# Performance work log

Hardware: AMD Instinct MI355X
Metric: run time of the kernel (lower is better)

Reference implementation:

```python
import jax, jax.numpy as jnp
import numpy as np

B, S, D = 1, 1024, 4096
N_HEADS, N_KV, HEAD_DIM = 32, 8, 128
ALPHA = 5.0
BUDGET = 0.2
NEG = -10000.0


def rotate_half(x):
    x1 = x[..., : x.shape[-1] // 2]
    x2 = x[..., x.shape[-1] // 2 :]
    return jnp.concatenate((-x2, x1), axis=-1)


def kv_cache_mask(scores):
    # scores: [b, h, T, S]. Faithful vectorized version of the torch per-row
    # topk/scatter loop (capacity=1.0 => eviction loop body never executes).
    b, h, T, Ssrc = scores.shape
    attn = scores.reshape(b * h, T, Ssrc)
    causal_add = jnp.triu(jnp.full((T, Ssrc), NEG, scores.dtype), 1)
    attn = attn + causal_add
    # torch: torch.max(attn, -1, keepdim=True)[0][0] -> row maxes of head 0 only
    max_val = jnp.max(attn[0], axis=-1, keepdims=True)  # [T, 1]
    fetch_num = jnp.sum(attn >= (max_val - ALPHA), axis=-1)  # [BH, T]
    fetch_num = jnp.mean(fetch_num.astype(scores.dtype), axis=0).astype(jnp.int32)  # [T]
    fetch_max = int(Ssrc * BUDGET)
    fetch_num = jnp.minimum(fetch_num, fetch_max)
    # rank of every column within its (row-causal-masked) row, descending score
    order = jnp.argsort(-attn, axis=-1)           # [BH, T, S]
    ranks = jnp.argsort(order, axis=-1)           # [BH, T, S]
    rows = jnp.arange(T)
    keep_topk = ranks < fetch_num[None, :, None]  # variable-k topk per row
    tril = jnp.arange(Ssrc)[None, :] <= rows[:, None]  # dense causal rows
    fetch = jnp.where((rows < fetch_max)[None, :, None], tril[None], keep_topk)
    mask = jnp.where(fetch, 0.0, NEG).astype(scores.dtype).reshape(b, h, T, Ssrc)
    density = fetch.astype(jnp.float32).sum() / (b * h) / (T * (T + 1) / 2)
    return mask, density


def setup_inputs() -> dict:
    key = jax.random.key(0)
    ks = jax.random.split(key, 5)
    hidden_states = jax.random.normal(ks[0], (B, S, D), jnp.float32)
    # standard RoPE tables, theta=10000
    inv_freq = 1.0 / (10000.0 ** (np.arange(0, HEAD_DIM, 2, dtype=np.float64) / HEAD_DIM))
    freqs = np.outer(np.arange(S, dtype=np.float64), inv_freq)  # [S, hd/2]
    emb = np.concatenate([freqs, freqs], axis=-1)               # [S, hd]
    cos = jnp.asarray(np.cos(emb), jnp.float32)[None]           # [1, S, hd]
    sin = jnp.asarray(np.sin(emb), jnp.float32)[None]
    Wq = jax.random.normal(ks[1], (N_HEADS * HEAD_DIM, D), jnp.float32) * 0.02
    Wk = jax.random.normal(ks[2], (N_KV * HEAD_DIM, D), jnp.float32) * 0.02
    Wv = jax.random.normal(ks[3], (N_KV * HEAD_DIM, D), jnp.float32) * 0.02
    Wo = jax.random.normal(ks[4], (D, N_HEADS * HEAD_DIM), jnp.float32) * 0.02
    return {"hidden_states": hidden_states, "cos": cos, "sin": sin,
            "Wq": Wq, "Wk": Wk, "Wv": Wv, "Wo": Wo}


def reference(hidden_states, cos, sin, Wq, Wk, Wv, Wo):
    b, s, d = hidden_states.shape
    scaling = HEAD_DIM ** -0.5
    q = (hidden_states @ Wq.T).reshape(b, s, N_HEADS, HEAD_DIM).transpose(0, 2, 1, 3)
    k = (hidden_states @ Wk.T).reshape(b, s, N_KV, HEAD_DIM).transpose(0, 2, 1, 3)
    v = (hidden_states @ Wv.T).reshape(b, s, N_KV, HEAD_DIM).transpose(0, 2, 1, 3)
    c = cos[:, None]  # [b, 1, s, hd]
    sn = sin[:, None]
    q = q * c + rotate_half(q) * sn
    k = k * c + rotate_half(k) * sn
    n_rep = N_HEADS // N_KV
    k = jnp.repeat(k, n_rep, axis=1)
    v = jnp.repeat(v, n_rep, axis=1)
    scores = jnp.einsum("bhqd,bhkd->bhqk", q, k) * scaling
    mask, _density = kv_cache_mask(scores)
    probs = jax.nn.softmax(scores + mask, axis=-1)
    out = jnp.einsum("bhqk,bhkd->bhqd", probs, v)
    out = out.transpose(0, 2, 1, 3).reshape(b, s, N_HEADS * HEAD_DIM)
    return out @ Wo.T
```

## Files before the change

kernel.cpp:

```cpp
#include <hip/hip_runtime.h>
#include <hip/hip_bf16.h>
#include <hip/hip_fp16.h>

typedef unsigned int u32;
typedef unsigned short u16;
typedef __bf16 bf16x8 __attribute__((ext_vector_type(8)));
typedef float floatx4 __attribute__((ext_vector_type(4)));

#define SCALE 0.08838834764831845f
#define FETCH_MAX 204

__device__ __forceinline__ float bf2f(u16 u) {
    union { u32 i; float f; } v; v.i = ((u32)u) << 16; return v.f;
}
__device__ __forceinline__ u16 f2bf(float f) {
    union { float f; u32 i; } v; v.f = f;
    u32 r = v.i + 0x7FFFu + ((v.i >> 16) & 1u);
    return (u16)(r >> 16);
}
__device__ __forceinline__ u16 f2h_bits(float f) {
    __half h = __float2half(f);
    union { __half h; u16 u; } v; v.h = h; return v.u;
}
__device__ __forceinline__ float h_bits2f(u16 u) {
    union { __half h; u16 u; } v; v.u = u; return __half2float(v.h);
}
__device__ __forceinline__ u32 h2key(u16 hb) {
    return (u32)(u16)(hb ^ ((hb & 0x8000u) ? 0xFFFFu : 0x8000u));
}
__device__ __forceinline__ u16 key2h(u32 k) {
    return (u16)((k & 0x8000u) ? (k ^ 0x8000u) : (k ^ 0xFFFFu));
}

__global__ void detect_k(const u32* cosw, int* flag) {
    if (threadIdx.x == 0 && blockIdx.x == 0)
        *flag = (cosw[0] == 0x3F800000u) ? 1 : 0;
}

__global__ __launch_bounds__(256) void zero_k(int* p, int n) {
    int i = blockIdx.x * 256 + threadIdx.x;
    if (i < n) p[i] = 0;
}

__global__ __launch_bounds__(256) void convert_k(
    const int* flagp, const float* hs, const float* wq, const float* wk,
    const float* wv, const float* wo,
    u16* chs, u16* cwq, u16* cwk, u16* cwv, u16* cwo)
{
    if (*flagp == 0) return;
    const long S0 = 4194304/4, S1 = 16777216/4, S2 = 4194304/4, S3 = 4194304/4, S4 = 16777216/4;
    const long total = S0+S1+S2+S3+S4;
    for (long idx = (long)blockIdx.x*256 + threadIdx.x; idx < total; idx += (long)gridDim.x*256) {
        const float* src; u16* dst; long o = idx;
        if (o < S0)            { src = hs; dst = chs; }
        else if ((o -= S0) < S1) { src = wq; dst = cwq; }
        else if ((o -= S1) < S2) { src = wk; dst = cwk; }
        else if ((o -= S2) < S3) { src = wv; dst = cwv; }
        else                   { o -= S3; src = wo; dst = cwo; }
        float4 v = ((const float4*)src)[o];
        u32 lo = (u32)f2bf(v.x) | ((u32)f2bf(v.y) << 16);
        u32 hi = (u32)f2bf(v.z) | ((u32)f2bf(v.w) << 16);
        ((uint2*)dst)[o] = make_uint2(lo, hi);
    }
}

__global__ __launch_bounds__(256) void gemm_bt(
    const int* flagp,
    const u16* A0, const u16* A1,
    const u16* B0a, const u16* B0b,
    const u16* B1a, const u16* B1b,
    const u16* B2a, const u16* B2b,
    int n0, int n1,
    u16* Cb, float* Cf,
    int M, int N, int K, int ldc)
{
    const int flag = *flagp;
    const u16* A  = flag ? A1 : A0;
    const u16* Bq = flag ? B0b : B0a;
    const u16* Bk = flag ? B1b : B1a;
    const u16* Bv = flag ? B2b : B2a;
    __shared__ u16 Al[128][72];
    __shared__ u16 Bl[128][72];
    const int tid = threadIdx.x;
    const int wave = tid >> 6, lane = tid & 63;
    const int qd = lane >> 4, l16 = lane & 15;
    const int wm = wave & 1, wn = wave >> 1;
    const int m0 = blockIdx.y * 128, nb = blockIdx.x * 128;
    floatx4 acc[4][4];
    floatx4 zf = {0.f, 0.f, 0.f, 0.f};
    for (int mt = 0; mt < 4; ++mt) for (int nt = 0; nt < 4; ++nt) acc[mt][nt] = zf;

    for (int k0 = 0; k0 < K; k0 += 64) {
        #pragma unroll
        for (int it = 0; it < 4; ++it) {
            int idx = tid + it*256;
            int r = idx >> 3, c8 = idx & 7;
            uint4 va = *(const uint4*)&A[(size_t)(m0 + r)*K + k0 + c8*8];
            *(uint4*)&Al[r][c8*8] = va;
            int f = nb + r;
            const u16* Brow = (f < n0) ? (Bq + (size_t)f*K)
                             : (f < n0 + n1) ? (Bk + (size_t)(f - n0)*K)
                             : (Bv + (size_t)(f - n0 - n1)*K);
            uint4 vb = *(const uint4*)&Brow[k0 + c8*8];
            *(uint4*)&Bl[r][c8*8] = vb;
        }
        __syncthreads();
        #pragma unroll
        for (int ks = 0; ks < 2; ++ks) {
            bf16x8 af[4], bfr[4];
            #pragma unroll
            for (int mt = 0; mt < 4; ++mt)
                af[mt] = *(const bf16x8*)&Al[wm*64 + mt*16 + l16][ks*32 + qd*8];
            #pragma unroll
            for (int nt = 0; nt < 4; ++nt)
                bfr[nt] = *(const bf16x8*)&Bl[wn*64 + nt*16 + l16][ks*32 + qd*8];
            #pragma unroll
            for (int mt = 0; mt < 4; ++mt)
                #pragma unroll
                for (int nt = 0; nt < 4; ++nt)
                    acc[mt][nt] = __builtin_amdgcn_mfma_f32_16x16x32_bf16(af[mt], bfr[nt], acc[mt][nt], 0, 0, 0);
        }
        __syncthreads();
    }
    const bool of32 = (Cf != nullptr) && flag;
    #pragma unroll
    for (int mt = 0; mt < 4; ++mt)
        #pragma unroll
        for (int nt = 0; nt < 4; ++nt)
            #pragma unroll
            for (int rg = 0; rg < 4; ++rg) {
                int row = m0 + wm*64 + mt*16 + qd*4 + rg;
                int col = nb + wn*64 + nt*16 + l16;
                float v = acc[mt][nt][rg];
                if (of32) Cf[(size_t)row*ldc + col] = v;
                else      Cb[(size_t)row*ldc + col] = f2bf(v);
            }
}

__global__ __launch_bounds__(256) void rope_k(const int* flagp, u16* QKV,
                                              const void* cosp, const void* sinp)
{
    const int flag = *flagp;
    long idx = (long)blockIdx.x*256 + threadIdx.x;
    int d = (int)(idx & 63);
    int t = (int)(idx >> 6);
    int slot = t % 40, i = t / 40;
    int col0 = (slot < 32) ? slot*128 : 4096 + (slot - 32)*128;
    size_t base = (size_t)i*6144 + col0;
    float q1 = bf2f(QKV[base + d]), q2 = bf2f(QKV[base + d + 64]);
    float c, s;
    if (flag) { c = ((const float*)cosp)[i*128 + d]; s = ((const float*)sinp)[i*128 + d]; }
    else      { c = bf2f(((const u16*)cosp)[i*128 + d]); s = bf2f(((const u16*)sinp)[i*128 + d]); }
    QKV[base + d]      = f2bf(q1*c - q2*s);
    QKV[base + d + 64] = f2bf(q2*c + q1*s);
}

__global__ __launch_bounds__(256) void vtrans_k(const u16* QKV, u16* VT)
{
    const int b = blockIdx.x;
    const int g = b >> 5, db = (b >> 4) & 1, jb = b & 15;
    __shared__ u16 t[64][72];
    const int tid = threadIdx.x;
    #pragma unroll
    for (int it = 0; it < 2; ++it) {
        int idx = tid + it*256;
        int jj = idx >> 3, c8 = idx & 7;
        uint4 v = *(const uint4*)&QKV[(size_t)(jb*64 + jj)*6144 + 5120 + g*128 + db*64 + c8*8];
        *(uint4*)&t[jj][c8*8] = v;
    }
    __syncthreads();
    #pragma unroll
    for (int it = 0; it < 2; ++it) {
        int idx = tid + it*256;
        int dd = idx >> 3, c8 = idx & 7;
        u16 tmp[8];
        #pragma unroll
        for (int e = 0; e < 8; ++e) tmp[e] = t[c8*8 + e][dd];
        *(uint4*)&VT[(size_t)(g*128 + db*64 + dd)*1024 + jb*64 + c8*8] = *(uint4*)tmp;
    }
}

__global__ __launch_bounds__(256) void rowmax0_k(const u16* QKV, float* rowmax0)
{
    const int i = blockIdx.x;
    __shared__ float Qs[128];
    __shared__ float wm4[4];
    const int tid = threadIdx.x, wave = tid >> 6, lane = tid & 63;
    if (tid < 16) {
        uint4 v = *(const uint4*)&QKV[(size_t)i*6144 + tid*8];
        Qs[tid*8+0] = bf2f((u16)(v.x & 0xffff)); Qs[tid*8+1] = bf2f((u16)(v.x >> 16));
        Qs[tid*8+2] = bf2f((u16)(v.y & 0xffff)); Qs[tid*8+3] = bf2f((u16)(v.y >> 16));
        Qs[tid*8+4] = bf2f((u16)(v.z & 0xffff)); Qs[tid*8+5] = bf2f((u16)(v.z >> 16));
        Qs[tid*8+6] = bf2f((u16)(v.w & 0xffff)); Qs[tid*8+7] = bf2f((u16)(v.w >> 16));
    }
    __syncthreads();
    float mx = -3.0e38f;
    for (int j = tid; j <= i; j += 256) {
        const u16* Kr = &QKV[(size_t)j*6144 + 4096];
        float acc = 0.f;
        #pragma unroll
        for (int c8 = 0; c8 < 16; ++c8) {
            uint4 v = *(const uint4*)&Kr[c8*8];
            acc += Qs[c8*8+0]*bf2f((u16)(v.x & 0xffff)) + Qs[c8*8+1]*bf2f((u16)(v.x >> 16));
            acc += Qs[c8*8+2]*bf2f((u16)(v.y & 0xffff)) + Qs[c8*8+3]*bf2f((u16)(v.y >> 16));
            acc += Qs[c8*8+4]*bf2f((u16)(v.z & 0xffff)) + Qs[c8*8+5]*bf2f((u16)(v.z >> 16));
            acc += Qs[c8*8+6]*bf2f((u16)(v.w & 0xffff)) + Qs[c8*8+7]*bf2f((u16)(v.w >> 16));
        }
        mx = fmaxf(mx, acc * SCALE);
    }
    #pragma unroll
    for (int off = 1; off < 64; off <<= 1) mx = fmaxf(mx, __shfl_xor(mx, off, 64));
    if (lane == 0) wm4[wave] = mx;
    __syncthreads();
    if (tid == 0) rowmax0[i] = fmaxf(fmaxf(wm4[0], wm4[1]), fmaxf(wm4[2], wm4[3]));
}

__global__ __launch_bounds__(256) void qk_count(
    const u16* QKV, const float* rowmax0, int* count_sum)
{
    const int bid = blockIdx.x;
    const int h = bid >> 6, rb = bid & 63;
    const int r0 = rb * 16, g = h >> 2;
    __shared__ u16 Kl[128][72];
    __shared__ u16 Ql[16][136];
    __shared__ int redcnt[4][16];
    const int tid = threadIdx.x, wave = tid >> 6, lane = tid & 63;
    const int qd = lane >> 4, l16 = lane & 15;
    {
        int r = tid >> 4, c8 = tid & 15;
        uint4 v = *(const uint4*)&QKV[(size_t)(r0 + r)*6144 + h*128 + c8*8];
        *(uint4*)&Ql[r][c8*8] = v;
    }
    __syncthreads();
    bf16x8 af[4];
    #pragma unroll
    for (int ks = 0; ks < 4; ++ks) af[ks] = *(const bf16x8*)&Ql[l16][ks*32 + qd*8];
    float rm0[4]; int runcnt[4];
    #pragma unroll
    for (int rg = 0; rg < 4; ++rg) {
        runcnt[rg] = 0;
        rm0[rg] = rowmax0[r0 + qd*4 + rg] - 5.0f;
    }
    const int jtiles = (r0 + 16 + 127) >> 7;
    for (int ct = 0; ct < jtiles; ++ct) {
        __syncthreads();
        #pragma unroll
        for (int it = 0; it < 8; ++it) {
            int idx = tid + it*256;
            int r = idx >> 4, c8 = idx & 15;
            uint4 v = *(const uint4*)&QKV[(size_t)(ct*128 + r)*6144 + 4096 + g*128 + c8*8];
            *(uint4*)&Kl[r][c8*8] = v;
        }
        __syncthreads();
        const int jw = wave * 32;
        #pragma unroll
        for (int nt = 0; nt < 2; ++nt) {
            floatx4 sa = {0.f, 0.f, 0.f, 0.f};
            #pragma unroll
            for (int ks = 0; ks < 4; ++ks) {
                bf16x8 bfr = *(const bf16x8*)&Kl[jw + nt*16 + l16][ks*32 + qd*8];
                sa = __builtin_amdgcn_mfma_f32_16x16x32_bf16(af[ks], bfr, sa, 0, 0, 0);
            }
            const int jc = ct*128 + jw + nt*16 + l16;
            #pragma unroll
            for (int rg = 0; rg < 4; ++rg) {
                float s = sa[rg] * SCALE;
                int i = r0 + qd*4 + rg;
                if (jc <= i) runcnt[rg] += (s >= rm0[rg]) ? 1 : 0;
            }
        }
    }
    #pragma unroll
    for (int off = 1; off < 16; off <<= 1)
        #pragma unroll
        for (int rg = 0; rg < 4; ++rg)
            runcnt[rg] += __shfl_xor(runcnt[rg], off, 64);
    if (l16 == 0)
        for (int rg = 0; rg < 4; ++rg)
            redcnt[wave][qd*4 + rg] = runcnt[rg];
    __syncthreads();
    if (tid < 16) {
        int c = redcnt[0][tid] + redcnt[1][tid] + redcnt[2][tid] + redcnt[3][tid];
        atomicAdd(&count_sum[r0 + tid], c);
    }
}

__global__ __launch_bounds__(256, 4) void select_attn(
    const u16* QKV, const u16* VT, const int* count_sum, u16* attn)
{
    const int bid = blockIdx.x;
    const int h = bid >> 6, rb = 63 - (bid & 63);
    const int r0 = rb * 16, g = h >> 2;
    const int tid = threadIdx.x, wave = tid >> 6, lane = tid & 63;
    const int qd = lane >> 4, l16 = lane & 15;
    __shared__ u16 SP[16][1032];
    __shared__ float denom[16];

    const int jtc = (r0 + 16 + 63) >> 6;

    bf16x8 af[4];
    #pragma unroll
    for (int ks = 0; ks < 4; ++ks)
        af[ks] = *(const bf16x8*)&QKV[(size_t)(r0 + l16)*6144 + h*128 + ks*32 + qd*8];

    #pragma unroll 2
    for (int ct = 0; ct < jtc; ++ct) {
        const int j = ct*64 + wave*16 + l16;
        floatx4 sa = {0.f, 0.f, 0.f, 0.f};
        #pragma unroll
        for (int ks = 0; ks < 4; ++ks) {
            bf16x8 bfr = *(const bf16x8*)&QKV[(size_t)j*6144 + 4096 + g*128 + ks*32 + qd*8];
            sa = __builtin_amdgcn_mfma_f32_16x16x32_bf16(af[ks], bfr, sa, 0, 0, 0);
        }
        #pragma unroll
        for (int rg = 0; rg < 4; ++rg)
            SP[qd*4 + rg][ct*64 + wave*16 + l16] = f2h_bits(sa[rg] * SCALE);
    }
    __syncthreads();

    for (int batch = 0; batch < 4; ++batch) {
        const int m = batch*4 + wave;
        const int i = r0 + m, n = i + 1;
        const bool full = (i < FETCH_MAX);

        u32 key[16];
        #pragma unroll
        for (int c = 0; c < 16; ++c) {
            u32 kk = 0u;
            if (c*64 < n) {
                int j = c*64 + lane;
                u32 t = h2key(SP[m][j]);
                kk = (j < n) ? t : 0u;
            }
            key[c] = kk;
        }

        u32 kmax = key[0];
        #pragma unroll
        for (int c = 1; c < 16; ++c) kmax = (key[c] > kmax) ? key[c] : kmax;
        #pragma unroll
        for (int off = 1; off < 64; off <<= 1) {
            u32 o = (u32)__shfl_xor((int)kmax, off, 64);
            kmax = (o > kmax) ? o : kmax;
        }
        const float rmax = h_bits2f(key2h(kmax));

        u32 Kstar = 0; int quota = 0;
        if (!full) {
            int k = count_sum[i] >> 5;
            if (k > FETCH_MAX) k = FETCH_MAX;
            if (k < 1) k = 1;
            u32 t = 0;
            #pragma unroll 1
            for (int bit = 15; bit >= 0; --bit) {
                u32 tc = t | (1u << bit);
                int cnt = 0;
                #pragma unroll
                for (int c = 0; c < 16; ++c)
                    if (c*64 < n)
                        cnt += __popcll(__ballot(key[c] >= tc));
                if (cnt >= k) t = tc;
            }
            Kstar = t;
            int cntgt = 0;
            #pragma unroll
            for (int c = 0; c < 16; ++c)
                if (c*64 < n)
                    cntgt += __popcll(__ballot(key[c] > Kstar));
            quota = k - cntgt;
        }

        float psum = 0.f; int eqbase = 0;
        #pragma unroll
        for (int c = 0; c < 16; ++c) {
            if (c < jtc) {
                float p = 0.f;
                if (c*64 < n) {
                    int j = c*64 + lane;
                    bool valid = (j < n);
                    bool keep;
                    if (full) keep = valid;
                    else {
                        bool eq = valid && (key[c] == Kstar);
                        unsigned long long em = __ballot(eq);
                        int rk = eqbase + __popcll(em & ((1ull << lane) - 1ull));
                        keep = valid && ((key[c] > Kstar) || (eq && rk < quota));
                        eqbase += __popcll(em);
                    }
                    if (keep) p = __expf(h_bits2f(key2h(key[c])) - rmax);
                }
                psum += p;
                SP[m][c*64 + lane] = f2bf(p);
            }
        }
        #pragma unroll
        for (int off = 1; off < 64; off <<= 1) psum += __shfl_xor(psum, off, 64);
        if (lane == 0) denom[m] = psum;
    }
    __syncthreads();

    floatx4 oacc[2];
    floatx4 zf = {0.f, 0.f, 0.f, 0.f};
    oacc[0] = zf; oacc[1] = zf;
    const u16* VTg = VT + (size_t)g*128*1024;
    #pragma unroll 2
    for (int jt = 0; jt < jtc; ++jt) {
        #pragma unroll
        for (int ks = 0; ks < 2; ++ks) {
            bf16x8 pa = *(const bf16x8*)&SP[l16][jt*64 + ks*32 + qd*8];
            #pragma unroll
            for (int nt = 0; nt < 2; ++nt) {
                bf16x8 bv = *(const bf16x8*)&VTg[(size_t)(wave*32 + nt*16 + l16)*1024 + jt*64 + ks*32 + qd*8];
                oacc[nt] = __builtin_amdgcn_mfma_f32_16x16x32_bf16(pa, bv, oacc[nt], 0, 0, 0);
            }
        }
    }
    #pragma unroll
    for (int nt = 0; nt < 2; ++nt)
        #pragma unroll
        for (int rg = 0; rg < 4; ++rg) {
            int m = qd*4 + rg;
            float v = oacc[nt][rg] / denom[m];
            attn[(size_t)(r0 + m)*4096 + (h << 7) + wave*32 + nt*16 + l16] = f2bf(v);
        }
}

extern "C" void kernel_launch(void* const* d_in, const int* in_sizes, int n_in,
                              void* d_out, int out_size, void* d_ws, size_t ws_size,
                              hipStream_t stream)
{
    const void* hs = d_in[0];
    const void* cs = d_in[1];
    const void* sn = d_in[2];
    const void* wq = d_in[3];
    const void* wk = d_in[4];
    const void* wv = d_in[5];
    const void* wo = d_in[6];
    (void)in_sizes; (void)n_in; (void)out_size; (void)ws_size;

    unsigned char* W = (unsigned char*)d_ws;
    int*    flag  = (int*)   (W);
    int*    cnt   = (int*)   (W + 256);
    float*  rmax0 = (float*) (W + 4608);
    u16*    qkv   = (u16*)   (W + 139776);
    u16*    attn  = (u16*)   (W + 12722688);
    u16*    chs   = (u16*)   (W + 21111296);
    u16*    cwq   = (u16*)   (W + 29499904);
    u16*    cwk   = (u16*)   (W + 63054336);
    u16*    cwv   = (u16*)   (W + 71442944);
    u16*    cwo   = (u16*)   (W + 79831552);
    u16*    vt    = (u16*)   (W + 21111296);

    detect_k<<<1, 64, 0, stream>>>((const u32*)cs, flag);
    convert_k<<<4096, 256, 0, stream>>>(flag, (const float*)hs, (const float*)wq,
                                        (const float*)wk, (const float*)wv, (const float*)wo,
                                        chs, cwq, cwk, cwv, cwo);
    gemm_bt<<<dim3(48, 8), 256, 0, stream>>>(flag,
        (const u16*)hs, chs,
        (const u16*)wq, cwq, (const u16*)wk, cwk, (const u16*)wv, cwv,
        4096, 1024, qkv, nullptr, 1024, 6144, 4096, 6144);
    vtrans_k<<<256, 256, 0, stream>>>(qkv, vt);
    rope_k<<<10240, 256, 0, stream>>>(flag, qkv, cs, sn);
    rowmax0_k<<<1024, 256, 0, stream>>>(qkv, rmax0);
    zero_k<<<4, 256, 0, stream>>>(cnt, 1024);
    qk_count<<<2048, 256, 0, stream>>>(qkv, rmax0, cnt);
    select_attn<<<2048, 256, 0, stream>>>(qkv, vt, cnt, attn);
    gemm_bt<<<dim3(32, 8), 256, 0, stream>>>(flag,
        attn, attn,
        (const u16*)wo, cwo, (const u16*)wo, cwo, (const u16*)wo, cwo,
        4096, 4096, (u16*)d_out, (float*)d_out, 1024, 4096, 4096, 4096);
}
```

Baseline: 605.7 us.

## Cache fp16 QK scores from counting kernel and reuse them in select_attn

The counting kernel now computes QK^T scores once in 64-column tiles, loading K directly from global memory instead of staging it in LDS. It counts threshold hits and also writes the fp16 scores to a packed, causal-triangular scratch buffer that reuses the converted-weight workspace. select_attn no longer recomputes the scores with MFMA; it copies its row block from that scratch into shared memory. This removes the duplicated QK matmul at the cost of roughly 35 MB of extra global writes and reads, and the scratch region overlaps buffers that must already be dead at that point.

```diff
diff --git a/kernel.cpp b/kernel.cpp
--- a/kernel.cpp
+++ b/kernel.cpp
@@ -215,59 +215,47 @@
     if (tid == 0) rowmax0[i] = fmaxf(fmaxf(wm4[0], wm4[1]), fmaxf(wm4[2], wm4[3]));
 }
 
-__global__ __launch_bounds__(256) void qk_count(
-    const u16* QKV, const float* rowmax0, int* count_sum)
+__global__ __launch_bounds__(256) void score_count(
+    const u16* QKV, const float* rowmax0, int* count_sum, u16* Sg)
 {
     const int bid = blockIdx.x;
-    const int h = bid >> 6, rb = bid & 63;
+    const int h = bid >> 6, rb = 63 - (bid & 63);
     const int r0 = rb * 16, g = h >> 2;
-    __shared__ u16 Kl[128][72];
-    __shared__ u16 Ql[16][136];
-    __shared__ int redcnt[4][16];
+    const int q4 = rb >> 2, rm4 = rb & 3;
+    const int jtc = q4 + 1;
+    const int jt64 = jtc * 64;
+    const size_t sbase = ((size_t)h*544 + (size_t)jtc*(2*q4 + rm4)) * 1024;
     const int tid = threadIdx.x, wave = tid >> 6, lane = tid & 63;
     const int qd = lane >> 4, l16 = lane & 15;
-    {
-        int r = tid >> 4, c8 = tid & 15;
-        uint4 v = *(const uint4*)&QKV[(size_t)(r0 + r)*6144 + h*128 + c8*8];
-        *(uint4*)&Ql[r][c8*8] = v;
-    }
-    __syncthreads();
+    __shared__ int redcnt[4][16];
+
     bf16x8 af[4];
     #pragma unroll
-    for (int ks = 0; ks < 4; ++ks) af[ks] = *(const bf16x8*)&Ql[l16][ks*32 + qd*8];
+    for (int ks = 0; ks < 4; ++ks)
+        af[ks] = *(const bf16x8*)&QKV[(size_t)(r0 + l16)*6144 + h*128 + ks*32 + qd*8];
+
     float rm0[4]; int runcnt[4];
     #pragma unroll
     for (int rg = 0; rg < 4; ++rg) {
         runcnt[rg] = 0;
         rm0[rg] = rowmax0[r0 + qd*4 + rg] - 5.0f;
     }
-    const int jtiles = (r0 + 16 + 127) >> 7;
-    for (int ct = 0; ct < jtiles; ++ct) {
-        __syncthreads();
-        #pragma unroll
-        for (int it = 0; it < 8; ++it) {
-            int idx = tid + it*256;
-            int r = idx >> 4, c8 = idx & 15;
-            uint4 v = *(const uint4*)&QKV[(size_t)(ct*128 + r)*6144 + 4096 + g*128 + c8*8];
-            *(uint4*)&Kl[r][c8*8] = v;
-        }
-        __syncthreads();
-        const int jw = wave * 32;
-        #pragma unroll
-        for (int nt = 0; nt < 2; ++nt) {
-            floatx4 sa = {0.f, 0.f, 0.f, 0.f};
-            #pragma unroll
-            for (int ks = 0; ks < 4; ++ks) {
-                bf16x8 bfr = *(const bf16x8*)&Kl[jw + nt*16 + l16][ks*32 + qd*8];
-                sa = __builtin_amdgcn_mfma_f32_16x16x32_bf16(af[ks], bfr, sa, 0, 0, 0);
-            }
-            const int jc = ct*128 + jw + nt*16 + l16;
-            #pragma unroll
-            for (int rg = 0; rg < 4; ++rg) {
-                float s = sa[rg] * SCALE;
-                int i = r0 + qd*4 + rg;
-                if (jc <= i) runcnt[rg] += (s >= rm0[rg]) ? 1 : 0;
-            }
+
+    #pragma unroll 2
+    for (int ct = 0; ct < jtc; ++ct) {
+        const int jc = ct*64 + wave*16 + l16;
+        floatx4 sa = {0.f, 0.f, 0.f, 0.f};
+        #pragma unroll
+        for (int ks = 0; ks < 4; ++ks) {
+            bf16x8 bfr = *(const bf16x8*)&QKV[(size_t)jc*6144 + 4096 + g*128 + ks*32 + qd*8];
+            sa = __builtin_amdgcn_mfma_f32_16x16x32_bf16(af[ks], bfr, sa, 0, 0, 0);
+        }
+        #pragma unroll
+        for (int rg = 0; rg < 4; ++rg) {
+            float s = sa[rg] * SCALE;
+            int i = r0 + qd*4 + rg;
+            if (jc <= i && s >= rm0[rg]) runcnt[rg]++;
+            Sg[sbase + (size_t)(qd*4 + rg)*jt64 + jc] = f2h_bits(s);
         }
     }
     #pragma unroll
@@ -276,6 +264,7 @@
         for (int rg = 0; rg < 4; ++rg)
             runcnt[rg] += __shfl_xor(runcnt[rg], off, 64);
     if (l16 == 0)
+        #pragma unroll
         for (int rg = 0; rg < 4; ++rg)
             redcnt[wave][qd*4 + rg] = runcnt[rg];
     __syncthreads();
@@ -286,35 +275,26 @@
 }
 
 __global__ __launch_bounds__(256, 4) void select_attn(
-    const u16* QKV, const u16* VT, const int* count_sum, u16* attn)
+    const u16* Sg, const u16* VT, const int* count_sum, u16* attn)
 {
     const int bid = blockIdx.x;
     const int h = bid >> 6, rb = 63 - (bid & 63);
     const int r0 = rb * 16, g = h >> 2;
+    const int q4 = rb >> 2, rm4 = rb & 3;
+    const int jtc = q4 + 1;
+    const int jt64 = jtc * 64;
+    const size_t sbase = ((size_t)h*544 + (size_t)jtc*(2*q4 + rm4)) * 1024;
     const int tid = threadIdx.x, wave = tid >> 6, lane = tid & 63;
     const int qd = lane >> 4, l16 = lane & 15;
     __shared__ u16 SP[16][1032];
     __shared__ float denom[16];
 
-    const int jtc = (r0 + 16 + 63) >> 6;
-
-    bf16x8 af[4];
-    #pragma unroll
-    for (int ks = 0; ks < 4; ++ks)
-        af[ks] = *(const bf16x8*)&QKV[(size_t)(r0 + l16)*6144 + h*128 + ks*32 + qd*8];
-
-    #pragma unroll 2
-    for (int ct = 0; ct < jtc; ++ct) {
-        const int j = ct*64 + wave*16 + l16;
-        floatx4 sa = {0.f, 0.f, 0.f, 0.f};
-        #pragma unroll
-        for (int ks = 0; ks < 4; ++ks) {
-            bf16x8 bfr = *(const bf16x8*)&QKV[(size_t)j*6144 + 4096 + g*128 + ks*32 + qd*8];
-            sa = __builtin_amdgcn_mfma_f32_16x16x32_bf16(af[ks], bfr, sa, 0, 0, 0);
-        }
-        #pragma unroll
-        for (int rg = 0; rg < 4; ++rg)
-            SP[qd*4 + rg][ct*64 + wave*16 + l16] = f2h_bits(sa[rg] * SCALE);
+    {
+        const int rl8 = jtc * 8;
+        for (int idx = tid; idx < 16*rl8; idx += 256) {
+            int m = idx / rl8, c = idx - m*rl8;
+            *(uint4*)&SP[m][c*8] = *(const uint4*)&Sg[sbase + (size_t)m*jt64 + c*8];
+        }
     }
     __syncthreads();
 
@@ -450,6 +430,7 @@
     u16*    cwv   = (u16*)   (W + 71442944);
     u16*    cwo   = (u16*)   (W + 79831552);
     u16*    vt    = (u16*)   (W + 21111296);
+    u16*    scrs  = (u16*)   (W + 29499904);
 
     detect_k<<<1, 64, 0, stream>>>((const u32*)cs, flag);
     convert_k<<<4096, 256, 0, stream>>>(flag, (const float*)hs, (const float*)wq,
@@ -463,8 +444,8 @@
     rope_k<<<10240, 256, 0, stream>>>(flag, qkv, cs, sn);
     rowmax0_k<<<1024, 256, 0, stream>>>(qkv, rmax0);
     zero_k<<<4, 256, 0, stream>>>(cnt, 1024);
-    qk_count<<<2048, 256, 0, stream>>>(qkv, rmax0, cnt);
-    select_attn<<<2048, 256, 0, stream>>>(qkv, vt, cnt, attn);
+    score_count<<<2048, 256, 0, stream>>>(qkv, rmax0, cnt, scrs);
+    select_attn<<<2048, 256, 0, stream>>>(scrs, vt, cnt, attn);
     gemm_bt<<<dim3(32, 8), 256, 0, stream>>>(flag,
         attn, attn,
         (const u16*)wo, cwo, (const u16*)wo, cwo, (const u16*)wo, cwo,
```

Measured after the change: 601.2 us. No clear change (-0.7%).
